# Kernel optimization log

Measured on AMD Instinct MI355X. Metric: run time of the kernel, lower is better.

## Reference

```python
import jax, jax.numpy as jnp
import numpy as np

NUM_EXPERTS = 16
HIDDEN_DIM = 1024
TOP_K = 4
INPUT_DIM = 4096
OUTPUT_DIM = 4096
BATCH = 4096


def setup_inputs() -> dict:
    key = jax.random.key(0)
    ks = jax.random.split(key, 6)
    total_cols = NUM_EXPERTS * HIDDEN_DIM
    return {
        "x": jax.random.normal(ks[0], (BATCH, INPUT_DIM), dtype=jnp.float32),
        "gate_w": jax.random.normal(ks[1], (INPUT_DIM, NUM_EXPERTS), dtype=jnp.float32) * 0.02,
        "gate_b": jnp.zeros((NUM_EXPERTS,), dtype=jnp.float32),
        "weight": jax.random.normal(ks[2], (INPUT_DIM, total_cols), dtype=jnp.float32) * 0.01,
        "agg_w": jax.random.normal(ks[3], (total_cols, OUTPUT_DIM), dtype=jnp.float32) * 0.02,
        "agg_b": jnp.zeros((OUTPUT_DIM,), dtype=jnp.float32),
    }


def reference(x, gate_w, gate_b, weight, agg_w, agg_b):
    # 1) gating logits (batch, E), 2) sum over batch -> (E,)
    gating_logits = x @ gate_w + gate_b
    gating_sum = gating_logits.sum(axis=0)
    # 3) global top-k expert selection -> binary mask over experts
    _, topk_inds = jax.lax.top_k(gating_sum, TOP_K)
    expert_mask = jnp.zeros((NUM_EXPERTS,), dtype=x.dtype).at[topk_inds].set(1.0)
    # 4/5) block-sparse matmul: mask replicated over all row blocks, so each
    # expert's column block [e*H:(e+1)*H] is x @ W_block if selected else 0.
    out_sparse = x @ weight  # (batch, E*H)
    col_mask = jnp.repeat(expert_mask, HIDDEN_DIM)  # (E*H,)
    out_sparse = out_sparse * col_mask[None, :]
    # 6) aggregator
    final_out = out_sparse @ agg_w + agg_b
    return final_out
```

## Files before the change

kernel.cpp:

```cpp
#include <hip/hip_runtime.h>
#include <hip/hip_bf16.h>


#define BATCH 4096
#define DIN 4096
#define NE 16
#define HD 1024
#define TOPK 4
#define TOTC (NE * HD)
#define NT 64

using bf16 = __hip_bfloat16;
typedef __attribute__((ext_vector_type(8))) short short8;
typedef __attribute__((ext_vector_type(4))) float f32x4;

__device__ inline short f2bs(float f) {
  __hip_bfloat16 h = __float2bfloat16(f);
  return *reinterpret_cast<short*>(&h);
}

__global__ void k_cvtsum(const float* __restrict__ x, bf16* __restrict__ xb,
                         float* __restrict__ colsum) {
  const int t = threadIdx.x;
  const int lane = t & 63;
  const int w = t >> 6;
  const int c = blockIdx.x * 256 + lane * 4;
  const int r0 = blockIdx.y * 128 + w * 32;
  float4 s = {0.f, 0.f, 0.f, 0.f};
  for (int i = 0; i < 32; ++i) {
    size_t off = (size_t)(r0 + i) * DIN + c;
    float4 v = *reinterpret_cast<const float4*>(x + off);
    s.x += v.x; s.y += v.y; s.z += v.z; s.w += v.w;
    ushort4 b;
    b.x = (unsigned short)f2bs(v.x); b.y = (unsigned short)f2bs(v.y);
    b.z = (unsigned short)f2bs(v.z); b.w = (unsigned short)f2bs(v.w);
    *reinterpret_cast<ushort4*>(reinterpret_cast<char*>(xb) + off * 2) = b;
  }
  __shared__ float sm[4][256];
  sm[w][lane * 4 + 0] = s.x; sm[w][lane * 4 + 1] = s.y;
  sm[w][lane * 4 + 2] = s.z; sm[w][lane * 4 + 3] = s.w;
  __syncthreads();
  float tot = sm[0][t] + sm[1][t] + sm[2][t] + sm[3][t];
  atomicAdd(&colsum[blockIdx.x * 256 + t], tot);
}

__global__ void k_gate(const float* __restrict__ colsum, const float* __restrict__ gw,
                       const float* __restrict__ gb, int* __restrict__ ids) {
  __shared__ float red[4][16];
  __shared__ float gs[16];
  int t = threadIdx.x;
  int e = t & 15, kg = t >> 4;
  float p = 0.f;
  for (int k = kg; k < DIN; k += 16) p += colsum[k] * gw[(size_t)k * NE + e];
  p += __shfl_down(p, 32);
  p += __shfl_down(p, 16);
  if ((t & 63) < 16) red[t >> 6][e] = p;
  __syncthreads();
  if (t < 16) gs[t] = red[0][t] + red[1][t] + red[2][t] + red[3][t] + (float)BATCH * gb[t];
  __syncthreads();
  if (t == 0) {
    float v[16];
    #pragma unroll
    for (int i = 0; i < 16; ++i) v[i] = gs[i];
    for (int j = 0; j < TOPK; ++j) {
      int bi = 0;
      float bv = v[0];
      for (int i2 = 1; i2 < 16; ++i2)
        if (v[i2] > bv) { bv = v[i2]; bi = i2; }
      ids[j] = bi;
      v[bi] = -3.4e38f;
    }
  }
}

__global__ void k_gather(const float* __restrict__ w, const float* __restrict__ a,
                         const int* __restrict__ ids,
                         bf16* __restrict__ wbt, bf16* __restrict__ abt) {
  __shared__ float tile[64 * 65];
  const int t = threadIdx.x;
  const int tc = t & 15, kr = t >> 4;
  const int tk = t & 7, nr0 = t >> 3;
  for (int tl = blockIdx.x; tl < 8192; tl += 2048) {
    const int wsel = tl < 4096;
    const int tidx = wsel ? tl : tl - 4096;
    const int k0 = (tidx & 63) * 64, n0 = (tidx >> 6) * 64;
    if (wsel) {
      const int e = ids[n0 >> 10];
      const int wc0 = e * HD + (n0 & 1023);
      #pragma unroll
      for (int j = 0; j < 4; ++j) {
        int kk = kr + j * 16;
        float4 v = *reinterpret_cast<const float4*>(w + (size_t)(k0 + kk) * TOTC + wc0 + tc * 4);
        float* dst = &tile[kk * 65 + tc * 4];
        dst[0] = v.x; dst[1] = v.y; dst[2] = v.z; dst[3] = v.w;
      }
    } else {
      const int e = ids[k0 >> 10];
      const int ar0 = e * HD + (k0 & 1023);
      #pragma unroll
      for (int j = 0; j < 4; ++j) {
        int kk = kr + j * 16;
        float4 v = *reinterpret_cast<const float4*>(a + (size_t)(ar0 + kk) * 4096 + n0 + tc * 4);
        float* dst = &tile[kk * 65 + tc * 4];
        dst[0] = v.x; dst[1] = v.y; dst[2] = v.z; dst[3] = v.w;
      }
    }
    __syncthreads();
    bf16* dstp = wsel ? wbt : abt;
    #pragma unroll
    for (int i = 0; i < 2; ++i) {
      int n = n0 + nr0 + i * 32;
      short8 r;
      #pragma unroll
      for (int m = 0; m < 8; ++m) r[m] = f2bs(tile[(tk * 8 + m) * 65 + nr0 + i * 32]);
      *reinterpret_cast<short8*>(dstp + (size_t)n * DIN + k0 + tk * 8) = r;
    }
    __syncthreads();
  }
}

#define MFMA_BF16 __builtin_amdgcn_mfma_f32_16x16x32_bf16
#define VM4 asm volatile("s_waitcnt vmcnt(4)" ::: "memory")
#define VM0 asm volatile("s_waitcnt vmcnt(0)" ::: "memory")
#define NOST ((void)0)

#define PH(BUF, Q, STG, GATE)                                                   \
  do {                                                                          \
    if ((Q) == 0) {                                                             \
      _Pragma("unroll") for (int nf = 0; nf < 4; ++nf) {                        \
        bfrag[nf][0] = LDB(BUF, nf, 0);                                         \
        bfrag[nf][1] = LDB(BUF, nf, 1);                                         \
      }                                                                         \
    }                                                                           \
    short8 aA0 = LDA(BUF, 2 * (Q), 0), aA1 = LDA(BUF, 2 * (Q), 1);              \
    short8 aB0 = LDA(BUF, 2 * (Q) + 1, 0), aB1 = LDA(BUF, 2 * (Q) + 1, 1);      \
    STG;                                                                        \
    GATE;                                                                       \
    __builtin_amdgcn_s_barrier();                                               \
    __builtin_amdgcn_s_setprio(1);                                              \
    _Pragma("unroll") for (int nf = 0; nf < 4; ++nf) {                          \
      acc[2 * (Q)][nf] = MFMA_BF16(aA0, bfrag[nf][0], acc[2 * (Q)][nf], 0, 0, 0);       \
      acc[2 * (Q)][nf] = MFMA_BF16(aA1, bfrag[nf][1], acc[2 * (Q)][nf], 0, 0, 0);       \
      acc[2 * (Q) + 1][nf] = MFMA_BF16(aB0, bfrag[nf][0], acc[2 * (Q) + 1][nf], 0, 0, 0); \
      acc[2 * (Q) + 1][nf] = MFMA_BF16(aB1, bfrag[nf][1], acc[2 * (Q) + 1][nf], 0, 0, 0); \
    }                                                                           \
    __builtin_amdgcn_s_setprio(0);                                              \
    __builtin_amdgcn_s_barrier();                                               \
  } while (0)

template <int STORE_F32>
__global__ __launch_bounds__(512, 2) void k_gemm8(
    const bf16* __restrict__ A, const bf16* __restrict__ Bt,
    bf16* __restrict__ Cb, float* __restrict__ Cf, const float* __restrict__ bias) {
  __shared__ __align__(16) char smraw[131072];
  const int t = threadIdx.x;
  const int lane = t & 63;
  const int w = t >> 6;
  const int wr = w >> 2;
  const int wc = w & 3;

  const int bid = blockIdx.x;
  const int xcd = bid & 7;
  const int i = bid >> 3;
  const int bm = ((xcd >> 1) * 4 + (i & 3)) * 256;
  const int bn = ((xcd & 1) * 8 + (i >> 2)) * 256;

  f32x4 acc[8][4] = {};
  short8 bfrag[4][2];

  const int srow = w * 16 + (lane >> 3);
  const int sgr = lane & 7;

  auto STAGE_A = [&](int buf, int half, int kt) {
    char* lb = smraw + buf * 65536 + half * 16384 + w * 2048 + lane * 16;
    #pragma unroll
    for (int i2 = 0; i2 < 2; ++i2) {
      int r = srow + i2 * 8;
      const bf16* g = A + (size_t)(bm + half * 128 + r) * 4096 + kt * 64 + ((sgr ^ (r & 7)) * 8);
      __builtin_amdgcn_global_load_lds(
          (const __attribute__((address_space(1))) void*)g,
          (__attribute__((address_space(3))) void*)(lb + i2 * 1024), 16, 0, 0);
    }
  };
  auto STAGE_B = [&](int buf, int half, int kt) {
    char* lb = smraw + buf * 65536 + 32768 + half * 16384 + w * 2048 + lane * 16;
    #pragma unroll
    for (int i2 = 0; i2 < 2; ++i2) {
      int r = srow + i2 * 8;
      const bf16* g = Bt + (size_t)(bn + half * 128 + r) * 4096 + kt * 64 + ((sgr ^ (r & 7)) * 8);
      __builtin_amdgcn_global_load_lds(
          (const __attribute__((address_space(1))) void*)g,
          (__attribute__((address_space(3))) void*)(lb + i2 * 1024), 16, 0, 0);
    }
  };
  auto LDA = [&](int buf, int mf, int kk) -> short8 {
    int r = mf * 16 + (lane & 15);
    int kb = ((kk * 4 + (lane >> 4)) ^ (r & 7)) * 16;
    return *reinterpret_cast<const short8*>(smraw + buf * 65536 + wr * 16384 + r * 128 + kb);
  };
  auto LDB = [&](int buf, int nf, int kk) -> short8 {
    int nc = wc * 64 + nf * 16 + (lane & 15);
    int half = nc >> 7, r = nc & 127;
    int kb = ((kk * 4 + (lane >> 4)) ^ (r & 7)) * 16;
    return *reinterpret_cast<const short8*>(smraw + buf * 65536 + 32768 + half * 16384 + r * 128 + kb);
  };

  STAGE_B(0, 0, 0); STAGE_B(0, 1, 0);
  STAGE_A(0, 0, 0); STAGE_A(0, 1, 0);
  STAGE_B(1, 0, 1); STAGE_B(1, 1, 1);
  VM4;
  __builtin_amdgcn_s_barrier();

  for (int tt = 0; tt < 31; ++tt) {
    const int a = 2 * tt;
    PH(0, 0, STAGE_A(1, 0, a + 1), NOST);
    PH(0, 1, STAGE_A(1, 1, a + 1), NOST);
    PH(0, 2, STAGE_B(0, 0, a + 2), NOST);
    PH(0, 3, STAGE_B(0, 1, a + 2), VM4);
    PH(1, 0, STAGE_A(0, 0, a + 2), NOST);
    PH(1, 1, STAGE_A(0, 1, a + 2), NOST);
    PH(1, 2, STAGE_B(1, 0, a + 3), NOST);
    PH(1, 3, STAGE_B(1, 1, a + 3), VM4);
  }
  PH(0, 0, STAGE_A(1, 0, 63), NOST);
  PH(0, 1, STAGE_A(1, 1, 63), NOST);
  PH(0, 2, NOST, NOST);
  PH(0, 3, NOST, VM0);
  PH(1, 0, NOST, NOST);
  PH(1, 1, NOST, NOST);
  PH(1, 2, NOST, NOST);
  PH(1, 3, NOST, NOST);

  const int cr = (lane >> 4) * 4;
  const int cc = lane & 15;
  #pragma unroll
  for (int mf = 0; mf < 8; ++mf) {
    #pragma unroll
    for (int nf = 0; nf < 4; ++nf) {
      int row = bm + wr * 128 + mf * 16 + cr;
      int col = bn + wc * 64 + nf * 16 + cc;
      #pragma unroll
      for (int r = 0; r < 4; ++r) {
        if constexpr (STORE_F32) {
          Cf[(size_t)(row + r) * 4096 + col] = acc[mf][nf][r] + bias[col];
        } else {
          Cb[(size_t)(row + r) * 4096 + col] = __float2bfloat16(acc[mf][nf][r]);
        }
      }
    }
  }
}

extern "C" void kernel_launch(void* const* d_in, const int* in_sizes, int n_in,
                              void* d_out, int out_size, void* d_ws, size_t ws_size,
                              hipStream_t stream) {
  const float* x = (const float*)d_in[0];
  const float* gate_w = (const float*)d_in[1];
  const float* gate_b = (const float*)d_in[2];
  const float* weight = (const float*)d_in[3];
  const float* agg_w = (const float*)d_in[4];
  const float* agg_b = (const float*)d_in[5];
  float* out = (float*)d_out;
  char* ws = (char*)d_ws;

  float* colsum = (float*)ws;
  int* ids = (int*)(ws + 16384);
  bf16* mid = (bf16*)(ws + (4u << 20));
  bf16* abt = (bf16*)(ws + (36u << 20));
  bf16* xb = (bf16*)d_out;
  bf16* wbt = (bf16*)((char*)d_out + (32u << 20));

  hipMemsetAsync(colsum, 0, DIN * sizeof(float), stream);
  k_cvtsum<<<dim3(16, 32), 256, 0, stream>>>(x, xb, colsum);
  k_gate<<<1, 256, 0, stream>>>(colsum, gate_w, gate_b, ids);
  k_gather<<<2048, 256, 0, stream>>>(weight, agg_w, ids, wbt, abt);
  k_gemm8<0><<<256, 512, 0, stream>>>(xb, wbt, mid, nullptr, nullptr);
  k_gemm8<1><<<256, 512, 0, stream>>>(mid, abt, nullptr, out, agg_b);
}
```

Before: 382.5 us.

## Switch GEMM to 4-wave blocks with 128x128 per-wave tiles and simpler double buffering

Replaces the 8-wave, 512-thread GEMM with a 4-wave, 256-thread kernel. Each wave now computes a 128x128 output tile (8x8 MFMA accumulators), which gives more register-level reuse of A and B fragments per LDS read. The pipeline is simplified to plain double buffering with a full vmcnt(0) wait every k-tile instead of the staggered vmcnt(4) scheme. The trade-off is a much higher register count per wave (256 accumulator floats), fewer waves to hide latency, and less overlap between loads and compute.

```diff
diff --git a/kernel.cpp b/kernel.cpp
--- a/kernel.cpp
+++ b/kernel.cpp
@@ -120,44 +120,36 @@
 }
 
 #define MFMA_BF16 __builtin_amdgcn_mfma_f32_16x16x32_bf16
-#define VM4 asm volatile("s_waitcnt vmcnt(4)" ::: "memory")
 #define VM0 asm volatile("s_waitcnt vmcnt(0)" ::: "memory")
 #define NOST ((void)0)
 
-#define PH(BUF, Q, STG, GATE)                                                   \
+#define PH(BUF, KK, STG, GATE)                                                  \
   do {                                                                          \
-    if ((Q) == 0) {                                                             \
-      _Pragma("unroll") for (int nf = 0; nf < 4; ++nf) {                        \
-        bfrag[nf][0] = LDB(BUF, nf, 0);                                         \
-        bfrag[nf][1] = LDB(BUF, nf, 1);                                         \
-      }                                                                         \
-    }                                                                           \
-    short8 aA0 = LDA(BUF, 2 * (Q), 0), aA1 = LDA(BUF, 2 * (Q), 1);              \
-    short8 aB0 = LDA(BUF, 2 * (Q) + 1, 0), aB1 = LDA(BUF, 2 * (Q) + 1, 1);      \
+    short8 bfr[8];                                                              \
+    _Pragma("unroll") for (int nf = 0; nf < 8; ++nf) bfr[nf] = LDB(BUF, nf, KK); \
     STG;                                                                        \
     GATE;                                                                       \
     __builtin_amdgcn_s_barrier();                                               \
     __builtin_amdgcn_s_setprio(1);                                              \
-    _Pragma("unroll") for (int nf = 0; nf < 4; ++nf) {                          \
-      acc[2 * (Q)][nf] = MFMA_BF16(aA0, bfrag[nf][0], acc[2 * (Q)][nf], 0, 0, 0);       \
-      acc[2 * (Q)][nf] = MFMA_BF16(aA1, bfrag[nf][1], acc[2 * (Q)][nf], 0, 0, 0);       \
-      acc[2 * (Q) + 1][nf] = MFMA_BF16(aB0, bfrag[nf][0], acc[2 * (Q) + 1][nf], 0, 0, 0); \
-      acc[2 * (Q) + 1][nf] = MFMA_BF16(aB1, bfrag[nf][1], acc[2 * (Q) + 1][nf], 0, 0, 0); \
+    _Pragma("unroll") for (int m = 0; m < 8; ++m) {                             \
+      short8 afr = LDA(BUF, m, KK);                                             \
+      _Pragma("unroll") for (int nf = 0; nf < 8; ++nf)                          \
+        acc[m][nf] = MFMA_BF16(afr, bfr[nf], acc[m][nf], 0, 0, 0);              \
     }                                                                           \
     __builtin_amdgcn_s_setprio(0);                                              \
     __builtin_amdgcn_s_barrier();                                               \
   } while (0)
 
 template <int STORE_F32>
-__global__ __launch_bounds__(512, 2) void k_gemm8(
+__global__ __launch_bounds__(256, 1) void k_gemm4(
     const bf16* __restrict__ A, const bf16* __restrict__ Bt,
     bf16* __restrict__ Cb, float* __restrict__ Cf, const float* __restrict__ bias) {
   __shared__ __align__(16) char smraw[131072];
   const int t = threadIdx.x;
   const int lane = t & 63;
   const int w = t >> 6;
-  const int wr = w >> 2;
-  const int wc = w & 3;
+  const int wr = w >> 1;
+  const int wc = w & 1;
 
   const int bid = blockIdx.x;
   const int xcd = bid & 7;
@@ -165,80 +157,65 @@
   const int bm = ((xcd >> 1) * 4 + (i & 3)) * 256;
   const int bn = ((xcd & 1) * 8 + (i >> 2)) * 256;
 
-  f32x4 acc[8][4] = {};
-  short8 bfrag[4][2];
-
-  const int srow = w * 16 + (lane >> 3);
-  const int sgr = lane & 7;
-
-  auto STAGE_A = [&](int buf, int half, int kt) {
-    char* lb = smraw + buf * 65536 + half * 16384 + w * 2048 + lane * 16;
-    #pragma unroll
-    for (int i2 = 0; i2 < 2; ++i2) {
-      int r = srow + i2 * 8;
-      const bf16* g = A + (size_t)(bm + half * 128 + r) * 4096 + kt * 64 + ((sgr ^ (r & 7)) * 8);
+  f32x4 acc[8][8] = {};
+
+  const int sr = t >> 3;
+  const int sg = t & 7;
+
+  auto STAGE_A = [&](int buf, int kt) {
+    #pragma unroll
+    for (int i2 = 0; i2 < 8; ++i2) {
+      int r = sr + i2 * 32;
+      const bf16* g = A + (size_t)(bm + r) * 4096 + kt * 64 + ((sg ^ (r & 7)) * 8);
       __builtin_amdgcn_global_load_lds(
           (const __attribute__((address_space(1))) void*)g,
-          (__attribute__((address_space(3))) void*)(lb + i2 * 1024), 16, 0, 0);
-    }
-  };
-  auto STAGE_B = [&](int buf, int half, int kt) {
-    char* lb = smraw + buf * 65536 + 32768 + half * 16384 + w * 2048 + lane * 16;
-    #pragma unroll
-    for (int i2 = 0; i2 < 2; ++i2) {
-      int r = srow + i2 * 8;
-      const bf16* g = Bt + (size_t)(bn + half * 128 + r) * 4096 + kt * 64 + ((sgr ^ (r & 7)) * 8);
+          (__attribute__((address_space(3))) void*)(smraw + buf * 65536 + r * 128 + sg * 16),
+          16, 0, 0);
+    }
+  };
+  auto STAGE_B = [&](int buf, int kt) {
+    #pragma unroll
+    for (int i2 = 0; i2 < 8; ++i2) {
+      int r = sr + i2 * 32;
+      const bf16* g = Bt + (size_t)(bn + r) * 4096 + kt * 64 + ((sg ^ (r & 7)) * 8);
       __builtin_amdgcn_global_load_lds(
           (const __attribute__((address_space(1))) void*)g,
-          (__attribute__((address_space(3))) void*)(lb + i2 * 1024), 16, 0, 0);
+          (__attribute__((address_space(3))) void*)(smraw + buf * 65536 + 32768 + r * 128 + sg * 16),
+          16, 0, 0);
     }
   };
   auto LDA = [&](int buf, int mf, int kk) -> short8 {
-    int r = mf * 16 + (lane & 15);
-    int kb = ((kk * 4 + (lane >> 4)) ^ (r & 7)) * 16;
-    return *reinterpret_cast<const short8*>(smraw + buf * 65536 + wr * 16384 + r * 128 + kb);
+    int r = wr * 128 + mf * 16 + (lane & 15);
+    int g = ((kk * 4 + (lane >> 4)) ^ (r & 7)) * 16;
+    return *reinterpret_cast<const short8*>(smraw + buf * 65536 + r * 128 + g);
   };
   auto LDB = [&](int buf, int nf, int kk) -> short8 {
-    int nc = wc * 64 + nf * 16 + (lane & 15);
-    int half = nc >> 7, r = nc & 127;
-    int kb = ((kk * 4 + (lane >> 4)) ^ (r & 7)) * 16;
-    return *reinterpret_cast<const short8*>(smraw + buf * 65536 + 32768 + half * 16384 + r * 128 + kb);
-  };
-
-  STAGE_B(0, 0, 0); STAGE_B(0, 1, 0);
-  STAGE_A(0, 0, 0); STAGE_A(0, 1, 0);
-  STAGE_B(1, 0, 1); STAGE_B(1, 1, 1);
-  VM4;
+    int r = wc * 128 + nf * 16 + (lane & 15);
+    int g = ((kk * 4 + (lane >> 4)) ^ (r & 7)) * 16;
+    return *reinterpret_cast<const short8*>(smraw + buf * 65536 + 32768 + r * 128 + g);
+  };
+
+  STAGE_A(0, 0);
+  STAGE_B(0, 0);
+  VM0;
   __builtin_amdgcn_s_barrier();
 
-  for (int tt = 0; tt < 31; ++tt) {
-    const int a = 2 * tt;
-    PH(0, 0, STAGE_A(1, 0, a + 1), NOST);
-    PH(0, 1, STAGE_A(1, 1, a + 1), NOST);
-    PH(0, 2, STAGE_B(0, 0, a + 2), NOST);
-    PH(0, 3, STAGE_B(0, 1, a + 2), VM4);
-    PH(1, 0, STAGE_A(0, 0, a + 2), NOST);
-    PH(1, 1, STAGE_A(0, 1, a + 2), NOST);
-    PH(1, 2, STAGE_B(1, 0, a + 3), NOST);
-    PH(1, 3, STAGE_B(1, 1, a + 3), VM4);
-  }
-  PH(0, 0, STAGE_A(1, 0, 63), NOST);
-  PH(0, 1, STAGE_A(1, 1, 63), NOST);
-  PH(0, 2, NOST, NOST);
-  PH(0, 3, NOST, VM0);
-  PH(1, 0, NOST, NOST);
-  PH(1, 1, NOST, NOST);
-  PH(1, 2, NOST, NOST);
-  PH(1, 3, NOST, NOST);
+  for (int j = 0; j < NT - 1; ++j) {
+    const int cur = j & 1, nxt = cur ^ 1;
+    PH(cur, 0, STAGE_A(nxt, j + 1), NOST);
+    PH(cur, 1, STAGE_B(nxt, j + 1), VM0);
+  }
+  PH((NT - 1) & 1, 0, NOST, NOST);
+  PH((NT - 1) & 1, 1, NOST, NOST);
 
   const int cr = (lane >> 4) * 4;
   const int cc = lane & 15;
   #pragma unroll
   for (int mf = 0; mf < 8; ++mf) {
     #pragma unroll
-    for (int nf = 0; nf < 4; ++nf) {
+    for (int nf = 0; nf < 8; ++nf) {
       int row = bm + wr * 128 + mf * 16 + cr;
-      int col = bn + wc * 64 + nf * 16 + cc;
+      int col = bn + wc * 128 + nf * 16 + cc;
       #pragma unroll
       for (int r = 0; r < 4; ++r) {
         if constexpr (STORE_F32) {
@@ -274,6 +251,6 @@
   k_cvtsum<<<dim3(16, 32), 256, 0, stream>>>(x, xb, colsum);
   k_gate<<<1, 256, 0, stream>>>(colsum, gate_w, gate_b, ids);
   k_gather<<<2048, 256, 0, stream>>>(weight, agg_w, ids, wbt, abt);
-  k_gemm8<0><<<256, 512, 0, stream>>>(xb, wbt, mid, nullptr, nullptr);
-  k_gemm8<1><<<256, 512, 0, stream>>>(mid, abt, nullptr, out, agg_b);
-}
+  k_gemm4<0><<<256, 256, 0, stream>>>(xb, wbt, mid, nullptr, nullptr);
+  k_gemm4<1><<<256, 256, 0, stream>>>(mid, abt, nullptr, out, agg_b);
+}
```

Measured after the change: 1.097 ms. 187% more time.
